# Performance work log

Measured on AMD Instinct MI355X. Metric: run time of the kernel, lower is better.

## Reference

```python
import jax, jax.numpy as jnp
import numpy as np

HIDDEN = 2048
KEY_DIM = 2048
NUM_HEADS = 16
EPS = 1e-05


def rms_norm(x, w, eps=EPS):
    ms = jnp.mean(x * x, axis=-1, keepdims=True)
    return x * jax.lax.rsqrt(ms + eps) * w


def setup_inputs() -> dict:
    key = jax.random.key(0)
    ks = jax.random.split(key, 6)
    bound = 1.0 / np.sqrt(HIDDEN)  # kaiming-uniform-ish scale
    x = jax.random.normal(ks[0], (2, 2048, HIDDEN), dtype=jnp.float32)
    rms_w = jnp.ones((HIDDEN,), dtype=jnp.float32)
    Wq = jax.random.uniform(ks[1], (HIDDEN, KEY_DIM), jnp.float32, -bound, bound)
    Wk = jax.random.uniform(ks[2], (HIDDEN, KEY_DIM), jnp.float32, -bound, bound)
    Wv = jax.random.uniform(ks[3], (HIDDEN, KEY_DIM), jnp.float32, -bound, bound)
    Wo = jax.random.uniform(ks[4], (KEY_DIM, HIDDEN), jnp.float32, -bound, bound)
    return {"x": x, "rms_w": rms_w, "Wq": Wq, "Wk": Wk, "Wv": Wv, "Wo": Wo}


def reference(x, rms_w, Wq, Wk, Wv, Wo):
    B, S, _ = x.shape
    residual = x
    xn = rms_norm(x, rms_w)
    # project and split heads: [B,S,H,Dh]
    q = (xn @ Wq).reshape(B, S, NUM_HEADS, KEY_DIM // NUM_HEADS)
    k = (xn @ Wk).reshape(B, S, NUM_HEADS, KEY_DIM // NUM_HEADS)
    v = (xn @ Wv).reshape(B, S, NUM_HEADS, KEY_DIM // NUM_HEADS)
    # NOTE: original scales by 1/sqrt(key_dim), not head_dim — kept faithful
    scale = 1.0 / jnp.sqrt(jnp.float32(KEY_DIM))
    scores = jnp.einsum('bshd,bthd->bhst', q, k) * scale  # [B,H,S,S]
    causal = jnp.tril(jnp.ones((S, S), dtype=bool))
    scores = jnp.where(causal[None, None], scores, -jnp.inf)
    probs = jax.nn.softmax(scores, axis=-1)  # stable max-subtract internally
    out = jnp.einsum('bhst,bthd->bshd', probs, v).reshape(B, S, KEY_DIM)
    return out @ Wo + residual
```

## Files before the change

kernel.cpp:

```cpp
#include <hip/hip_runtime.h>
#include <math.h>

typedef __attribute__((ext_vector_type(8))) short bf16x8;
typedef __attribute__((ext_vector_type(4))) float f32x4;
typedef __attribute__((ext_vector_type(16))) float f32x16;

#define HID 2048
#define SEQ 2048
#define NH  16
#define DH  128
#define QK_SCALE 0.02209708691207961f

__device__ __forceinline__ ushort f2bf(float f) {
  union { float f; unsigned u; } v; v.f = f;
  unsigned r = v.u + 0x7fffu + ((v.u >> 16) & 1u);
  return (ushort)(r >> 16);
}

__device__ __forceinline__ void gload16(const ushort* g, ushort* l) {
  __builtin_amdgcn_global_load_lds((const __attribute__((address_space(1))) void*)g,
                                   (__attribute__((address_space(3))) void*)l,
                                   16, 0, 0);
}

__global__ __launch_bounds__(256) void k_transpose4(const float* __restrict__ W0,
                                                    const float* __restrict__ W1,
                                                    const float* __restrict__ W2,
                                                    const float* __restrict__ W3,
                                                    ushort* __restrict__ T0,
                                                    ushort* __restrict__ T3) {
  __shared__ float t[32][33];
  int z = blockIdx.z;
  const float* W = (z == 0) ? W0 : (z == 1) ? W1 : (z == 2) ? W2 : W3;
  ushort* Wt = (z == 3) ? T3 : (T0 + (size_t)z * 2048 * 2048);
  int n0 = blockIdx.x * 32, k0 = blockIdx.y * 32;
  int tx = threadIdx.x, ty = threadIdx.y;
  for (int i = ty; i < 32; i += 8)
    t[i][tx] = W[(size_t)(k0 + i) * HID + n0 + tx];
  __syncthreads();
  for (int i = ty; i < 32; i += 8)
    Wt[(size_t)(n0 + i) * HID + k0 + tx] = f2bf(t[tx][i]);
}

__global__ __launch_bounds__(256) void k_rmsnorm(const float* __restrict__ x,
                                                 const float* __restrict__ w,
                                                 ushort* __restrict__ xn) {
  int row = blockIdx.x;
  const float* xr = x + (size_t)row * HID;
  int base = threadIdx.x * 8;
  float4 a = *(const float4*)(xr + base);
  float4 c = *(const float4*)(xr + base + 4);
  float ss = a.x*a.x + a.y*a.y + a.z*a.z + a.w*a.w
           + c.x*c.x + c.y*c.y + c.z*c.z + c.w*c.w;
  #pragma unroll
  for (int off = 32; off > 0; off >>= 1) ss += __shfl_xor(ss, off);
  __shared__ float red[4];
  if ((threadIdx.x & 63) == 0) red[threadIdx.x >> 6] = ss;
  __syncthreads();
  float tot = red[0] + red[1] + red[2] + red[3];
  float sc = rsqrtf(tot * (1.0f / HID) + 1e-5f);
  float4 wa = *(const float4*)(w + base);
  float4 wc = *(const float4*)(w + base + 4);
  ushort h[8];
  h[0] = f2bf(a.x * sc * wa.x); h[1] = f2bf(a.y * sc * wa.y);
  h[2] = f2bf(a.z * sc * wa.z); h[3] = f2bf(a.w * sc * wa.w);
  h[4] = f2bf(c.x * sc * wc.x); h[5] = f2bf(c.y * sc * wc.y);
  h[6] = f2bf(c.z * sc * wc.z); h[7] = f2bf(c.w * sc * wc.w);
  int4 pk;
  pk.x = h[0] | ((int)h[1] << 16);
  pk.y = h[2] | ((int)h[3] << 16);
  pk.z = h[4] | ((int)h[5] << 16);
  pk.w = h[6] | ((int)h[7] << 16);
  *(int4*)&xn[(size_t)row * HID + base] = pk;
}

template <int MODE>
__global__ __launch_bounds__(256) void k_gemm7(const ushort* __restrict__ A,
                                               const ushort* __restrict__ Bt,
                                               ushort* __restrict__ obf,
                                               ushort* __restrict__ vt,
                                               float* __restrict__ ofl,
                                               const float* __restrict__ resid,
                                               int K) {
  __shared__ ushort sA[128 * 64];
  __shared__ ushort sB[128 * 64];
  const int tid = threadIdx.x;
  const int lane = tid & 63, w = tid >> 6;
  const int wr = w >> 1, wc = w & 1;
  const int bm = blockIdx.y, bn = blockIdx.x;
  const int g = lane >> 4, l15 = lane & 15;
  f32x4 acc[4][4];
  #pragma unroll
  for (int i = 0; i < 4; ++i)
    #pragma unroll
    for (int j = 0; j < 4; ++j) acc[i][j] = f32x4{0.f, 0.f, 0.f, 0.f};

  const ushort* ap[4];
  const ushort* bp[4];
  ushort* la[4];
  ushort* lb[4];
  #pragma unroll
  for (int c = 0; c < 4; ++c) {
    int id = (w * 4 + c) * 64 + lane;
    int r = id >> 3, ck = id & 7;
    int ke = (ck ^ (r & 7)) * 8;
    ap[c] = &A[(size_t)(bm * 128 + r) * K + ke];
    bp[c] = &Bt[(size_t)(bn * 128 + r) * K + ke];
    la[c] = ((ushort*)sA) + (w * 4 + c) * 512;
    lb[c] = ((ushort*)sB) + (w * 4 + c) * 512;
  }

  const int nt = K / 64;
  #pragma unroll 1
  for (int t = 0; t < nt; ++t) {
    #pragma unroll
    for (int c = 0; c < 4; ++c) {
      gload16(ap[c], la[c]);
      gload16(bp[c], lb[c]);
      ap[c] += 64;
      bp[c] += 64;
    }
    __syncthreads();
    #pragma unroll
    for (int kk = 0; kk < 2; ++kk) {
      bf16x8 aF[4], bF[4];
      #pragma unroll
      for (int i = 0; i < 4; ++i) {
        int row = wr * 64 + i * 16 + l15;
        int cp = (kk * 4 + g) ^ (lane & 7);
        aF[i] = *(const bf16x8*)&sA[row * 64 + cp * 8];
      }
      #pragma unroll
      for (int j = 0; j < 4; ++j) {
        int row = wc * 64 + j * 16 + l15;
        int cp = (kk * 4 + g) ^ (lane & 7);
        bF[j] = *(const bf16x8*)&sB[row * 64 + cp * 8];
      }
      #pragma unroll
      for (int i = 0; i < 4; ++i)
        #pragma unroll
        for (int j = 0; j < 4; ++j)
          acc[i][j] = __builtin_amdgcn_mfma_f32_16x16x32_bf16(aF[i], bF[j], acc[i][j], 0, 0, 0);
    }
    __syncthreads();
  }

  int rbase = bm * 128 + wr * 64 + g * 4;
  int cbase = bn * 128 + wc * 64 + l15;
  #pragma unroll
  for (int i = 0; i < 4; ++i) {
    #pragma unroll
    for (int j = 0; j < 4; ++j) {
      int col = cbase + j * 16;
      #pragma unroll
      for (int r = 0; r < 4; ++r) {
        int row = rbase + i * 16 + r;
        float v = acc[i][j][r];
        if (MODE == 0) {
          ushort hv = f2bf(v);
          if (col < 4096) {
            obf[(size_t)row * 4096 + col] = hv;
          } else {
            int nv = col - 4096;
            int h = nv >> 7, d = nv & 127;
            int b = row >> 11, s = row & 2047;
            vt[(size_t)((b * NH + h) * DH + d) * SEQ + s] = hv;
          }
        } else {
          ofl[(size_t)row * HID + col] = v + resid[(size_t)row * HID + col];
        }
      }
    }
  }
}

__global__ __launch_bounds__(256, 2) void k_attn4(const ushort* __restrict__ qk,
                                                  const ushort* __restrict__ vt,
                                                  ushort* __restrict__ aout) {
  __shared__ ushort sK[64 * 128];
  __shared__ ushort sV[128 * 64];
  const int tid = threadIdx.x;
  const int lane = tid & 63, w = tid >> 6;
  const int h2 = lane >> 5;
  const int l31 = lane & 31;
  const int bid = blockIdx.x;
  const int t = bid >> 3;
  const int bh = (bid & 7) + 8 * (t >> 4);
  const int qblk = 15 - (t & 15);
  const int b = bh >> 4, hh = bh & 15;
  const int q0w = qblk * 128 + w * 32;

  bf16x8 qf[8];
  {
    const ushort* qbase = qk + (size_t)(b * SEQ + q0w + l31) * 4096 + hh * DH;
    #pragma unroll
    for (int kk = 0; kk < 8; ++kk) qf[kk] = *(const bf16x8*)&qbase[kk * 16 + h2 * 8];
  }

  const ushort* kp[4];
  const ushort* vp[4];
  ushort* lk[4];
  ushort* lv[4];
  #pragma unroll
  for (int c = 0; c < 4; ++c) {
    int id = (w * 4 + c) * 64 + lane;
    int kr = id >> 4, ck = id & 15;
    kp[c] = qk + (size_t)(b * SEQ + kr) * 4096 + 2048 + hh * DH + ((ck ^ (kr & 7)) * 8);
    int dr = id >> 3, cv = id & 7;
    vp[c] = vt + (size_t)(bh * DH + dr) * SEQ + ((cv ^ (dr & 7)) * 8);
    lk[c] = ((ushort*)sK) + (size_t)(w * 4 + c) * 512;
    lv[c] = ((ushort*)sV) + (size_t)(w * 4 + c) * 512;
  }

  f32x16 accO[4];
  #pragma unroll
  for (int i = 0; i < 4; ++i)
    #pragma unroll
    for (int r = 0; r < 16; ++r) accO[i][r] = 0.f;
  float m_r = -1e30f, l_r = 0.f;

  const int ntile = 2 * qblk + 2;
  #pragma unroll 1
  for (int tt = 0; tt < ntile; ++tt) {
    const int t0 = tt * 64;
    #pragma unroll
    for (int c = 0; c < 4; ++c) {
      gload16(kp[c], lk[c]);
      gload16(vp[c], lv[c]);
      kp[c] += 64 * 4096;
      vp[c] += 64;
    }
    __syncthreads();

    if (t0 <= q0w + 31) {
      f32x16 accS[2];
      #pragma unroll
      for (int i = 0; i < 2; ++i)
        #pragma unroll
        for (int r = 0; r < 16; ++r) accS[i][r] = 0.f;
      #pragma unroll
      for (int kt = 0; kt < 2; ++kt) {
        const int row = kt * 32 + l31;
        #pragma unroll
        for (int kk = 0; kk < 8; ++kk) {
          const int cp = (kk * 2 + h2) ^ (lane & 7);
          bf16x8 kf = *(const bf16x8*)&sK[row * 128 + cp * 8];
          accS[kt] = __builtin_amdgcn_mfma_f32_32x32x16_bf16(kf, qf[kk], accS[kt], 0, 0, 0);
        }
      }
      const int qa = q0w + l31;
      float pmax = -INFINITY;
      if (t0 + 63 <= q0w) {
        #pragma unroll
        for (int kt = 0; kt < 2; ++kt)
          #pragma unroll
          for (int r = 0; r < 16; ++r) {
            float s = accS[kt][r] * QK_SCALE;
            accS[kt][r] = s;
            pmax = fmaxf(pmax, s);
          }
      } else {
        #pragma unroll
        for (int kt = 0; kt < 2; ++kt)
          #pragma unroll
          for (int r = 0; r < 16; ++r) {
            int ka = t0 + kt * 32 + (r & 3) + 8 * (r >> 2) + 4 * h2;
            float s = (ka <= qa) ? accS[kt][r] * QK_SCALE : -INFINITY;
            accS[kt][r] = s;
            pmax = fmaxf(pmax, s);
          }
      }
      pmax = fmaxf(pmax, __shfl_xor(pmax, 32));
      if (__any(pmax > m_r + 8.f)) {
        float mn = fmaxf(m_r, pmax);
        float al = __expf(m_r - mn);
        m_r = mn;
        l_r *= al;
        #pragma unroll
        for (int r = 0; r < 16; ++r) {
          float ar = __shfl(al, (r & 3) + 8 * (r >> 2) + 4 * h2);
          #pragma unroll
          for (int ds = 0; ds < 4; ++ds) accO[ds][r] *= ar;
        }
      }
      float rs = 0.f;
      #pragma unroll
      for (int kt = 0; kt < 2; ++kt)
        #pragma unroll
        for (int r = 0; r < 16; ++r) {
          float p = __expf(accS[kt][r] - m_r);
          rs += p;
          accS[kt][r] = p;
        }
      rs += __shfl_xor(rs, 32);
      l_r += rs;
      uint W[2][4][2];
      #pragma unroll
      for (int kt = 0; kt < 2; ++kt)
        #pragma unroll
        for (int bq = 0; bq < 4; ++bq)
          #pragma unroll
          for (int w2 = 0; w2 < 2; ++w2) {
            uint u0 = __float_as_uint(accS[kt][bq * 4 + w2 * 2]);
            uint u1 = __float_as_uint(accS[kt][bq * 4 + w2 * 2 + 1]);
            W[kt][bq][w2] = (u0 >> 16) | (u1 & 0xffff0000u);
          }
      #pragma unroll
      for (int kc = 0; kc < 4; ++kc) {
        const int kt = kc >> 1, pq = kc & 1;
        uint X0 = W[kt][2 * pq][0],     X1 = W[kt][2 * pq][1];
        uint Y0 = W[kt][2 * pq + 1][0], Y1 = W[kt][2 * pq + 1][1];
        uint sx0 = (uint)__shfl_xor((int)X0, 32);
        uint sx1 = (uint)__shfl_xor((int)X1, 32);
        uint sy0 = (uint)__shfl_xor((int)Y0, 32);
        uint sy1 = (uint)__shfl_xor((int)Y1, 32);
        union { uint u[4]; bf16x8 v; } pu;
        pu.u[0] = h2 ? sy0 : X0;
        pu.u[1] = h2 ? sy1 : X1;
        pu.u[2] = h2 ? Y0 : sx0;
        pu.u[3] = h2 ? Y1 : sx1;
        #pragma unroll
        for (int ds = 0; ds < 4; ++ds) {
          const int dr = ds * 32 + l31;
          const int cp = (kc * 2 + h2) ^ (lane & 7);
          bf16x8 vf = *(const bf16x8*)&sV[dr * 64 + cp * 8];
          accO[ds] = __builtin_amdgcn_mfma_f32_32x32x16_bf16(pu.v, vf, accO[ds], 0, 0, 0);
        }
      }
    }
    __syncthreads();
  }

  float linv = 1.f / l_r;
  #pragma unroll
  for (int r = 0; r < 16; ++r) {
    int qrel = (r & 3) + 8 * (r >> 2) + 4 * h2;
    float li = __shfl(linv, qrel);
    #pragma unroll
    for (int ds = 0; ds < 4; ++ds) {
      aout[(size_t)(b * SEQ + q0w + qrel) * HID + hh * DH + ds * 32 + l31] =
          f2bf(accO[ds][r] * li);
    }
  }
}

extern "C" void kernel_launch(void* const* d_in, const int* in_sizes, int n_in,
                              void* d_out, int out_size, void* d_ws, size_t ws_size,
                              hipStream_t stream) {
  const float* x     = (const float*)d_in[0];
  const float* rms_w = (const float*)d_in[1];
  const float* Wq    = (const float*)d_in[2];
  const float* Wk    = (const float*)d_in[3];
  const float* Wv    = (const float*)d_in[4];
  const float* Wo    = (const float*)d_in[5];
  float* out = (float*)d_out;

  char* ws = (char*)d_ws;
  ushort* WqkvT = (ushort*)ws; ws += (size_t)6144 * 2048 * 2;
  ushort* WoT   = (ushort*)ws; ws += (size_t)2048 * 2048 * 2;
  ushort* xn    = (ushort*)ws; ws += (size_t)4096 * 2048 * 2;
  ushort* qkbuf = (ushort*)ws; ws += (size_t)4096 * 4096 * 2;
  ushort* vt    = (ushort*)ws; ws += (size_t)4096 * 2048 * 2;
  ushort* aout  = (ushort*)ws; ws += (size_t)4096 * 2048 * 2;

  k_transpose4<<<dim3(64, 64, 4), dim3(32, 8), 0, stream>>>(Wq, Wk, Wv, Wo, WqkvT, WoT);

  k_rmsnorm<<<4096, 256, 0, stream>>>(x, rms_w, xn);

  k_gemm7<0><<<dim3(48, 32), 256, 0, stream>>>(xn, WqkvT, qkbuf, vt, nullptr, nullptr, 2048);

  k_attn4<<<512, 256, 0, stream>>>(qkbuf, vt, aout);

  k_gemm7<1><<<dim3(16, 32), 256, 0, stream>>>(aout, WoT, nullptr, nullptr, out, x, 2048);
}
```

Measured before the change: 299.1 us.

## Replace QKV GEMM with 256x256-tile, 8-wave, double-buffered pipelined kernel

```diff
diff --git a/kernel.cpp b/kernel.cpp
--- a/kernel.cpp
+++ b/kernel.cpp
@@ -22,6 +22,9 @@
                                    (__attribute__((address_space(3))) void*)l,
                                    16, 0, 0);
 }
+
+#define VMCNT(n) asm volatile("s_waitcnt vmcnt(" #n ")" ::: "memory")
+#define ABAR()   asm volatile("s_barrier" ::: "memory")
 
 __global__ __launch_bounds__(256) void k_transpose4(const float* __restrict__ W0,
                                                     const float* __restrict__ W1,
@@ -74,14 +77,151 @@
   *(int4*)&xn[(size_t)row * HID + base] = pk;
 }
 
-template <int MODE>
-__global__ __launch_bounds__(256) void k_gemm7(const ushort* __restrict__ A,
-                                               const ushort* __restrict__ Bt,
-                                               ushort* __restrict__ obf,
-                                               ushort* __restrict__ vt,
-                                               float* __restrict__ ofl,
-                                               const float* __restrict__ resid,
-                                               int K) {
+__global__ __launch_bounds__(512, 2) void k_gemm8(const ushort* __restrict__ A,
+                                                  const ushort* __restrict__ Bt,
+                                                  ushort* __restrict__ obf,
+                                                  ushort* __restrict__ vt) {
+  constexpr int K = 2048, NT = 32;
+  __shared__ ushort lds[2][4][128 * 64];
+  const int tid = threadIdx.x;
+  const int lane = tid & 63, w = tid >> 6;
+  const int wm = w >> 2, wn = w & 3;
+  const int g = lane >> 4, l15 = lane & 15;
+  const int bm = blockIdx.y, bn = blockIdx.x;
+  const int regB = 2 + (wn >> 1);
+  const int pbi = wm * 2 + (wn & 1);
+  const int lrow8 = lane >> 3;
+  const int ksw = ((lane & 7) ^ lrow8) * 8;
+
+  f32x4 acc[8][4];
+  #pragma unroll
+  for (int i = 0; i < 8; ++i)
+    #pragma unroll
+    for (int j = 0; j < 4; ++j) acc[i][j] = f32x4{0.f, 0.f, 0.f, 0.f};
+
+  const ushort* pa[4];
+  const ushort* pb[4];
+  #pragma unroll
+  for (int L = 0; L < 4; ++L) {
+    pa[L] = &A[(size_t)(bm * 256 + wm * 128 + (wn * 4 + L) * 8 + lrow8) * K + ksw];
+    pb[L] = &Bt[(size_t)(bn * 256 + (wn >> 1) * 128 + (pbi * 4 + L) * 8 + lrow8) * K + ksw];
+  }
+
+  bf16x8 aLo[4][2], aHi[4][2], b01[2][2], b23[2][2];
+
+  auto LDAlo = [&](int buf) {
+    #pragma unroll
+    for (int i = 0; i < 4; ++i)
+      #pragma unroll
+      for (int kk = 0; kk < 2; ++kk)
+        aLo[i][kk] = *(const bf16x8*)&lds[buf][wm][(i * 16 + l15) * 64 +
+                                                   (((kk * 4 + g) ^ (lane & 7)) * 8)];
+  };
+  auto LDAhi = [&](int buf) {
+    #pragma unroll
+    for (int i = 0; i < 4; ++i)
+      #pragma unroll
+      for (int kk = 0; kk < 2; ++kk)
+        aHi[i][kk] = *(const bf16x8*)&lds[buf][wm][((i + 4) * 16 + l15) * 64 +
+                                                   (((kk * 4 + g) ^ (lane & 7)) * 8)];
+  };
+  auto LDB = [&](bf16x8 (*dst)[2], int buf, int jb) {
+    #pragma unroll
+    for (int j = 0; j < 2; ++j)
+      #pragma unroll
+      for (int kk = 0; kk < 2; ++kk)
+        dst[j][kk] = *(const bf16x8*)&lds[buf][regB][((wn & 1) * 64 + (jb + j) * 16 + l15) * 64 +
+                                                     (((kk * 4 + g) ^ (lane & 7)) * 8)];
+  };
+  auto STA = [&](int buf, int L) {
+    gload16(pa[L], &lds[buf][wm][(wn * 4 + L) * 512]);
+    pa[L] += 64;
+  };
+  auto STB = [&](int buf, int L) {
+    gload16(pb[L], &lds[buf][regB][(pbi * 4 + L) * 512]);
+    pb[L] += 64;
+  };
+  auto MM = [&](bf16x8 (*a)[2], bf16x8 (*b)[2], int i0, int j0) {
+    __builtin_amdgcn_s_setprio(1);
+    #pragma unroll
+    for (int i = 0; i < 4; ++i)
+      #pragma unroll
+      for (int j = 0; j < 2; ++j)
+        #pragma unroll
+        for (int kk = 0; kk < 2; ++kk)
+          acc[i0 + i][j0 + j] = __builtin_amdgcn_mfma_f32_16x16x32_bf16(
+              a[i][kk], b[j][kk], acc[i0 + i][j0 + j], 0, 0, 0);
+    __builtin_amdgcn_s_setprio(0);
+  };
+
+  STA(0, 0); STA(0, 1); STA(0, 2); STA(0, 3);
+  STB(0, 0); STB(0, 1); STB(0, 2); STB(0, 3);
+  VMCNT(4); ABAR();
+
+  #pragma unroll 1
+  for (int t = 0; t < NT - 1; ++t) {
+    const int buf = t & 1, nbuf = buf ^ 1;
+    LDAlo(buf);
+    STA(nbuf, 0); STA(nbuf, 1);
+    VMCNT(2); ABAR();
+    LDB(b01, buf, 0);
+    MM(aLo, b01, 0, 0);
+    ABAR();
+    LDB(b23, buf, 2);
+    STA(nbuf, 2); STA(nbuf, 3);
+    ABAR();
+    MM(aLo, b23, 0, 2);
+    ABAR();
+    LDAhi(buf);
+    STB(nbuf, 0); STB(nbuf, 1);
+    ABAR();
+    MM(aHi, b23, 4, 2);
+    ABAR();
+    STB(nbuf, 2); STB(nbuf, 3);
+    VMCNT(4); ABAR();
+    MM(aHi, b01, 4, 0);
+    ABAR();
+  }
+  LDAlo(1);
+  VMCNT(0); ABAR();
+  LDB(b01, 1, 0);
+  MM(aLo, b01, 0, 0);
+  LDB(b23, 1, 2);
+  MM(aLo, b23, 0, 2);
+  LDAhi(1);
+  MM(aHi, b23, 4, 2);
+  MM(aHi, b01, 4, 0);
+
+  int rbase = bm * 256 + wm * 128 + g * 4;
+  int cbase = bn * 256 + wn * 64 + l15;
+  #pragma unroll
+  for (int i = 0; i < 8; ++i) {
+    #pragma unroll
+    for (int j = 0; j < 4; ++j) {
+      int col = cbase + j * 16;
+      #pragma unroll
+      for (int r = 0; r < 4; ++r) {
+        int row = rbase + i * 16 + r;
+        float v = acc[i][j][r];
+        ushort hv = f2bf(v);
+        if (col < 4096) {
+          obf[(size_t)row * 4096 + col] = hv;
+        } else {
+          int nv = col - 4096;
+          int h = nv >> 7, d = nv & 127;
+          int b = row >> 11, s = row & 2047;
+          vt[(size_t)((b * NH + h) * DH + d) * SEQ + s] = hv;
+        }
+      }
+    }
+  }
+}
+
+__global__ __launch_bounds__(256) void k_gemm7o(const ushort* __restrict__ A,
+                                                const ushort* __restrict__ Bt,
+                                                float* __restrict__ ofl,
+                                                const float* __restrict__ resid,
+                                                int K) {
   __shared__ ushort sA[128 * 64];
   __shared__ ushort sB[128 * 64];
   const int tid = threadIdx.x;
@@ -155,20 +295,7 @@
       #pragma unroll
       for (int r = 0; r < 4; ++r) {
         int row = rbase + i * 16 + r;
-        float v = acc[i][j][r];
-        if (MODE == 0) {
-          ushort hv = f2bf(v);
-          if (col < 4096) {
-            obf[(size_t)row * 4096 + col] = hv;
-          } else {
-            int nv = col - 4096;
-            int h = nv >> 7, d = nv & 127;
-            int b = row >> 11, s = row & 2047;
-            vt[(size_t)((b * NH + h) * DH + d) * SEQ + s] = hv;
-          }
-        } else {
-          ofl[(size_t)row * HID + col] = v + resid[(size_t)row * HID + col];
-        }
+        ofl[(size_t)row * HID + col] = acc[i][j][r] + resid[(size_t)row * HID + col];
       }
     }
   }
@@ -367,9 +494,9 @@
 
   k_rmsnorm<<<4096, 256, 0, stream>>>(x, rms_w, xn);
 
-  k_gemm7<0><<<dim3(48, 32), 256, 0, stream>>>(xn, WqkvT, qkbuf, vt, nullptr, nullptr, 2048);
+  k_gemm8<<<dim3(24, 16), 512, 0, stream>>>(xn, WqkvT, qkbuf, vt);
 
   k_attn4<<<512, 256, 0, stream>>>(qkbuf, vt, aout);
 
-  k_gemm7<1><<<dim3(16, 32), 256, 0, stream>>>(aout, WoT, nullptr, nullptr, out, x, 2048);
-}
+  k_gemm7o<<<dim3(16, 32), 256, 0, stream>>>(aout, WoT, out, x, 2048);
+}
```

New measurement: 297.9 us. Within noise of the previous version (-0.4%).
